# Kernel optimization log

Measured on AMD Instinct MI355X. Metric: run time of the kernel, lower is better.

Reference implementation:

```python
import jax, jax.numpy as jnp
import numpy as np
import math

N_HEAD = 8
LN_EPS = 1e-5


def _layernorm(x, w, b):
    # Biased variance as in the triton kernel: var = E[x^2] - mean^2
    mean = jnp.mean(x, axis=-1, keepdims=True)
    var = jnp.mean(x * x, axis=-1, keepdims=True) - mean * mean
    return (x - mean) * jax.lax.rsqrt(var + LN_EPS) * w + b


def _gelu_tanh(x):
    # matches triton gelu: tanh approximation
    return 0.5 * x * (1.0 + jnp.tanh(0.7978845608 * (x + 0.044715 * x * x * x)))


def _causal_attention(qkv, n_head):
    B, T, C3 = qkv.shape
    C = C3 // 3
    D = C // n_head
    q, k, v = jnp.split(qkv, 3, axis=-1)
    q = q.reshape(B, T, n_head, D)
    k = k.reshape(B, T, n_head, D)
    v = v.reshape(B, T, n_head, D)
    scale = 1.0 / math.sqrt(D)
    scores = jnp.einsum('bqhd,bkhd->bhqk', q, k) * scale  # [B,H,T,T]
    causal = jnp.tril(jnp.ones((T, T), dtype=bool))
    scores = jnp.where(causal, scores, -jnp.inf)
    p = jax.nn.softmax(scores, axis=-1)
    out = jnp.einsum('bhqk,bkhd->bqhd', p, v)
    return out.reshape(B, T, C)


def setup_inputs() -> dict:
    key = jax.random.key(0)
    ks = jax.random.split(key, 8)
    B, T, C = 8, 2048, 768
    s = 0.02
    return {
        'x': jax.random.normal(ks[0], (B, T, C), jnp.float32),
        'ln1_w': jnp.ones((C,), jnp.float32),
        'ln1_b': jnp.zeros((C,), jnp.float32),
        'w_qkv': jax.random.normal(ks[1], (3 * C, C), jnp.float32) * s,
        'b_qkv': jnp.zeros((3 * C,), jnp.float32),
        'w_attn_proj': jax.random.normal(ks[2], (C, C), jnp.float32) * s,
        'b_attn_proj': jnp.zeros((C,), jnp.float32),
        'ln2_w': jnp.ones((C,), jnp.float32),
        'ln2_b': jnp.zeros((C,), jnp.float32),
        'w_fc': jax.random.normal(ks[3], (4 * C, C), jnp.float32) * s,
        'b_fc': jnp.zeros((4 * C,), jnp.float32),
        'w_mlp_proj': jax.random.normal(ks[4], (C, 4 * C), jnp.float32) * s,
        'b_mlp_proj': jnp.zeros((C,), jnp.float32),
    }


def reference(x, ln1_w, ln1_b, w_qkv, b_qkv, w_attn_proj, b_attn_proj,
              ln2_w, ln2_b, w_fc, b_fc, w_mlp_proj, b_mlp_proj):
    # attention block: fused LN + QKV linear, causal flash attention, out proj, residual
    qkv = _layernorm(x, ln1_w, ln1_b) @ w_qkv.T + b_qkv          # [B,T,3C]
    att = _causal_attention(qkv, N_HEAD)                          # [B,T,C]
    x = x + (att @ w_attn_proj.T + b_attn_proj)
    # MLP block: fused LN + fc + gelu, proj, residual
    h = _gelu_tanh(_layernorm(x, ln2_w, ln2_b) @ w_fc.T + b_fc)   # [B,T,4C]
    x = x + (h @ w_mlp_proj.T + b_mlp_proj)
    return x
```

## Files before the change

kernel.cpp:

```cpp
#include <hip/hip_runtime.h>
#include <hip/hip_bf16.h>
#include <cstdint>
#include <cstddef>

typedef __attribute__((ext_vector_type(8))) short bf16x8;
typedef __attribute__((ext_vector_type(4))) short bf16x4;
typedef __attribute__((ext_vector_type(4))) float f32x4;
typedef __attribute__((ext_vector_type(16))) float f32x16;

#define GLB_AS(p) ((const __attribute__((address_space(1))) void*)(p))
#define LDS_AS(p) ((__attribute__((address_space(3))) void*)(p))

__device__ __forceinline__ short f2bf(float f) {
    union { float f; unsigned u; } x; x.f = f;
    unsigned r = (x.u + 0x7fffu + ((x.u >> 16) & 1u)) >> 16;
    return (short)r;
}
__device__ __forceinline__ unsigned packbf2(float a, float b) {
    union { float f; unsigned u; } x, y; x.f = a; y.f = b;
    return (x.u >> 16) | (y.u & 0xffff0000u);
}
__device__ __forceinline__ f32x4 MF(bf16x8 a, bf16x8 b, f32x4 c) {
    return __builtin_amdgcn_mfma_f32_16x16x32_bf16(a, b, c, 0, 0, 0);
}
__device__ __forceinline__ f32x16 MF32(bf16x8 a, bf16x8 b, f32x16 c) {
    return __builtin_amdgcn_mfma_f32_32x32x16_bf16(a, b, c, 0, 0, 0);
}

__global__ __launch_bounds__(256) void k_cast4(const float* __restrict__ s0,
                                               const float* __restrict__ s1,
                                               const float* __restrict__ s2,
                                               const float* __restrict__ s3,
                                               short* __restrict__ d0,
                                               short* __restrict__ d1,
                                               short* __restrict__ d2,
                                               short* __restrict__ d3,
                                               int n0, int n1, int n2, int n3) {
    const int total = n0 + n1 + n2 + n3;
    int i = blockIdx.x * 256 + threadIdx.x;
    const int stride = gridDim.x * 256;
    for (; i < total; i += stride) {
        int j = i;
        const float* s; short* d;
        if (j < n0) { s = s0; d = d0; }
        else {
            j -= n0;
            if (j < n1) { s = s1; d = d1; }
            else {
                j -= n1;
                if (j < n2) { s = s2; d = d2; }
                else { j -= n2; s = s3; d = d3; }
            }
        }
        float4 v = ((const float4*)s)[j];
        bf16x4 o;
        o[0] = f2bf(v.x); o[1] = f2bf(v.y); o[2] = f2bf(v.z); o[3] = f2bf(v.w);
        ((bf16x4*)d)[j] = o;
    }
}

__global__ __launch_bounds__(256) void k_layernorm(const float* __restrict__ x,
                                                   const float* __restrict__ w,
                                                   const float* __restrict__ b,
                                                   short* __restrict__ out) {
    const int row = blockIdx.x;
    const int tid = threadIdx.x;
    const float* xr = x + (size_t)row * 768;
    float v0 = xr[tid], v1 = xr[tid + 256], v2 = xr[tid + 512];
    float s = v0 + v1 + v2;
    float ss = v0 * v0 + v1 * v1 + v2 * v2;
    #pragma unroll
    for (int m = 32; m; m >>= 1) { s += __shfl_xor(s, m); ss += __shfl_xor(ss, m); }
    __shared__ float red[8];
    int wid = tid >> 6, lane = tid & 63;
    if (lane == 0) { red[wid] = s; red[4 + wid] = ss; }
    __syncthreads();
    s = red[0] + red[1] + red[2] + red[3];
    ss = red[4] + red[5] + red[6] + red[7];
    float mean = s * (1.f / 768.f);
    float var = ss * (1.f / 768.f) - mean * mean;
    float inv = rsqrtf(var + 1e-5f);
    short* orow = out + (size_t)row * 768;
    orow[tid]       = f2bf((v0 - mean) * inv * w[tid]       + b[tid]);
    orow[tid + 256] = f2bf((v1 - mean) * inv * w[tid + 256] + b[tid + 256]);
    orow[tid + 512] = f2bf((v2 - mean) * inv * w[tid + 512] + b[tid + 512]);
}

template <int EPI, int NFR>
__global__ __launch_bounds__(512, 2) void k_gemm256(const short* __restrict__ A,
                                                    const short* __restrict__ B,
                                                    const float* __restrict__ bias,
                                                    const float* __restrict__ res,
                                                    void* __restrict__ out,
                                                    int M, int N, int K) {
    __shared__ short As2[2][256 * 64];
    __shared__ short Bs2[2][NFR * 64 * 64];
    const int tid = threadIdx.x, lane = tid & 63, wid = tid >> 6;
    const int l4 = lane & 15, lh = lane >> 4;
    const int wm = wid >> 2, wn = wid & 3;
    const int gx = gridDim.x;
    const int nwg = gx * gridDim.y;
    int wg = blockIdx.y * gx + blockIdx.x;
    { const int q = nwg >> 3; wg = (wg & 7) * q + (wg >> 3); }
    const int row0 = (wg / gx) * 256, col0 = (wg % gx) * (NFR * 64);

    auto stageA = [&](short* lds, int mh, int k0) {
        #pragma unroll
        for (int i = 0; i < 2; ++i) {
            const int chunk = wid * 2 + i;
            const int dl = mh * 16384 + chunk * 1024 + lane * 16;
            const int r = dl >> 7;
            const int cb = (dl & 127) ^ ((r & 7) << 4);
            __builtin_amdgcn_global_load_lds(
                GLB_AS(A + (size_t)(row0 + r) * K + k0 + (cb >> 1)),
                LDS_AS(lds + mh * 8192 + chunk * 512), 16, 0, 0);
        }
    };
    auto stageB = [&](short* lds, int k0) {
        #pragma unroll
        for (int i = 0; i < NFR; ++i) {
            const int chunk = wid * NFR + i;
            const int dl = chunk * 1024 + lane * 16;
            const int r = dl >> 7;
            const int cb = (dl & 127) ^ ((r & 7) << 4);
            __builtin_amdgcn_global_load_lds(
                GLB_AS(B + (size_t)(col0 + r) * K + k0 + (cb >> 1)),
                LDS_AS(lds + chunk * 512), 16, 0, 0);
        }
    };
    auto rd = [&](const short* lds, int r, int kb) -> bf16x8 {
        return *(const bf16x8*)((const char*)lds + r * 128 +
                                ((kb * 64 + lh * 16) ^ ((r & 7) << 4)));
    };

    f32x4 acc[8][NFR] = {};
    bf16x8 a[4][2], b0[2][2], b1[2][2];
    const int NT = K >> 6;

    stageA(As2[0], 0, 0);
    stageA(As2[0], 1, 0);
    stageB(Bs2[0], 0);
    asm volatile("s_waitcnt vmcnt(0)" ::: "memory");
    __builtin_amdgcn_s_barrier();

    for (int t = 0; t < NT; ++t) {
        const int cur = t & 1, nxt = cur ^ 1;
        const short* Ac = As2[cur];
        const short* Bc = Bs2[cur];
        const int kn = (t + 1) << 6;
        const bool more = (t + 1 < NT);
        #pragma unroll
        for (int mi = 0; mi < 4; ++mi) {
            const int r = wm * 128 + mi * 16 + l4;
            a[mi][0] = rd(Ac, r, 0); a[mi][1] = rd(Ac, r, 1);
        }
        #pragma unroll
        for (int ni = 0; ni < 2; ++ni) {
            const int r = wn * (NFR * 16) + ni * 16 + l4;
            b0[ni][0] = rd(Bc, r, 0); b0[ni][1] = rd(Bc, r, 1);
        }
        if (more) { stageA(As2[nxt], 0, kn); stageA(As2[nxt], 1, kn); }
        __builtin_amdgcn_s_setprio(1);
        #pragma unroll
        for (int mi = 0; mi < 4; ++mi)
            #pragma unroll
            for (int ni = 0; ni < 2; ++ni) {
                acc[mi][ni] = MF(a[mi][0], b0[ni][0], acc[mi][ni]);
                acc[mi][ni] = MF(a[mi][1], b0[ni][1], acc[mi][ni]);
            }
        __builtin_amdgcn_s_setprio(0);
        __builtin_amdgcn_s_barrier();
        #pragma unroll
        for (int j = 0; j < NFR - 2; ++j) {
            const int r = wn * (NFR * 16) + (2 + j) * 16 + l4;
            b1[j][0] = rd(Bc, r, 0); b1[j][1] = rd(Bc, r, 1);
        }
        if (more) stageB(Bs2[nxt], kn);
        __builtin_amdgcn_s_setprio(1);
        #pragma unroll
        for (int mi = 0; mi < 4; ++mi)
            #pragma unroll
            for (int j = 0; j < NFR - 2; ++j) {
                acc[mi][2 + j] = MF(a[mi][0], b1[j][0], acc[mi][2 + j]);
                acc[mi][2 + j] = MF(a[mi][1], b1[j][1], acc[mi][2 + j]);
            }
        __builtin_amdgcn_s_setprio(0);
        __builtin_amdgcn_s_barrier();
        #pragma unroll
        for (int mi = 0; mi < 4; ++mi) {
            const int r = wm * 128 + (4 + mi) * 16 + l4;
            a[mi][0] = rd(Ac, r, 0); a[mi][1] = rd(Ac, r, 1);
        }
        __builtin_amdgcn_s_setprio(1);
        #pragma unroll
        for (int mi = 0; mi < 4; ++mi)
            #pragma unroll
            for (int j = 0; j < NFR - 2; ++j) {
                acc[4 + mi][2 + j] = MF(a[mi][0], b1[j][0], acc[4 + mi][2 + j]);
                acc[4 + mi][2 + j] = MF(a[mi][1], b1[j][1], acc[4 + mi][2 + j]);
            }
        __builtin_amdgcn_s_setprio(0);
        __builtin_amdgcn_s_barrier();
        __builtin_amdgcn_s_setprio(1);
        #pragma unroll
        for (int mi = 0; mi < 4; ++mi)
            #pragma unroll
            for (int ni = 0; ni < 2; ++ni) {
                acc[4 + mi][ni] = MF(a[mi][0], b0[ni][0], acc[4 + mi][ni]);
                acc[4 + mi][ni] = MF(a[mi][1], b0[ni][1], acc[4 + mi][ni]);
            }
        __builtin_amdgcn_s_setprio(0);
        asm volatile("s_waitcnt vmcnt(0)" ::: "memory");
        __builtin_amdgcn_s_barrier();
    }

    #pragma unroll
    for (int mi = 0; mi < 8; ++mi) {
        const int rowb = row0 + wm * 128 + mi * 16 + lh * 4;
        #pragma unroll
        for (int ni = 0; ni < NFR; ++ni) {
            const int col = col0 + wn * (NFR * 16) + ni * 16 + l4;
            const float bv = bias[col];
            #pragma unroll
            for (int j = 0; j < 4; ++j) {
                const size_t idx = (size_t)(rowb + j) * N + col;
                float v = acc[mi][ni][j] + bv;
                if (EPI == 0) {
                    ((short*)out)[idx] = f2bf(v);
                } else if (EPI == 1) {
                    ((float*)out)[idx] = v + res[idx];
                } else {
                    float u = v + 0.044715f * v * v * v;
                    float t = 1.f - 2.f / (__expf(1.5957691216f * u) + 1.f);
                    ((short*)out)[idx] = f2bf(0.5f * v * (1.f + t));
                }
            }
        }
    }
}

__global__ __launch_bounds__(256, 2) void k_attn6(const short* __restrict__ qkv,
                                                  short* __restrict__ att) {
    __shared__ short Ks[2][64 * 128];
    __shared__ short Vs[2][96 * 64];
    const int tid = threadIdx.x, lane = tid & 63, wid = tid >> 6;
    const int lq = lane & 31, hi = lane >> 5;
    const int h = blockIdx.y, b = blockIdx.z;
    const short* base = qkv + (size_t)b * 2048 * 2304 + h * 96;
    const short* Kb = base + 768;
    const short* Vb = base + 1536;
    const int vkvr = (tid / 12) * 4, vd0 = (tid % 12) * 8;
    const int vslot = (vkvr & ~12) | ((vkvr & 4) << 1) | ((vkvr & 8) >> 1);
    bf16x8 vreg[4];
    const float QSC = 0.14724445f;

    auto stageK = [&](int jt, int bb) {
        const int kv0 = jt * 64;
        for (int c = wid; c < 16; c += 4) {
            const int dl = c * 1024 + lane * 16;
            const int row = dl >> 8;
            const int scol = (dl & 255) ^ ((row & 7) << 4);
            __builtin_amdgcn_global_load_lds(GLB_AS(Kb + (size_t)(kv0 + row) * 2304 + (scol >> 1)),
                                             LDS_AS(&Ks[bb][c * 512]), 16, 0, 0);
        }
    };
    auto loadV = [&](int jt) {
        if (tid < 192) {
            const int kv0 = jt * 64;
            #pragma unroll
            for (int e = 0; e < 4; ++e)
                vreg[e] = *(const bf16x8*)(Vb + (size_t)(kv0 + vkvr + e) * 2304 + vd0);
        }
    };
    auto writeV = [&](int bb) {
        if (tid < 192) {
            #pragma unroll
            for (int f = 0; f < 8; ++f) {
                const int row = vd0 + f;
                const int sw = ((row & 7) ^ ((row >> 3) & 7)) << 4;
                const int byte = (row * 128 + vslot * 2) ^ sw;
                bf16x4 w4;
                w4[0] = vreg[0][f]; w4[1] = vreg[1][f]; w4[2] = vreg[2][f]; w4[3] = vreg[3][f];
                *(bf16x4*)((char*)&Vs[bb][0] + byte) = w4;
            }
        }
    };

    for (int half = 0; half < 2; ++half) {
        const int qt = half ? 15 - (int)blockIdx.x : (int)blockIdx.x;
        const int q0 = qt * 128 + wid * 32;
        const int qa = q0 + lq;

        bf16x8 qf[6];
        #pragma unroll
        for (int kb = 0; kb < 6; ++kb) {
            bf16x8 v = *(const bf16x8*)(base + (size_t)qa * 2304 + kb * 16 + hi * 8);
            #pragma unroll
            for (int e = 0; e < 8; ++e) {
                union { unsigned u; float f; } x;
                x.u = ((unsigned)(unsigned short)v[e]) << 16;
                qf[kb][e] = f2bf(x.f * QSC);
            }
        }

        f32x16 o[3] = {};
        float lrow = 0.f;
        const int nt = 2 * qt + 2;

        stageK(0, 0);
        loadV(0);
        asm volatile("s_waitcnt vmcnt(0)" ::: "memory");
        writeV(0);
        __syncthreads();

        int cur = 0;
        for (int jt = 0; jt < nt; ++jt) {
            const int nxt = cur ^ 1;
            const bool more = (jt + 1 < nt);
            if (more) { stageK(jt + 1, nxt); loadV(jt + 1); }

            const int kv0 = jt * 64;
            if (kv0 <= q0 + 31) {
                const bool full = (kv0 + 63 <= q0);
                f32x16 s0 = {}, s1 = {};
                #pragma unroll
                for (int kb = 0; kb < 6; ++kb) {
                    const int r0 = lq, r1 = 32 + lq;
                    bf16x8 kf0 = *(const bf16x8*)((const char*)&Ks[cur][0] +
                                  r0 * 256 + ((kb * 32 + hi * 16) ^ ((r0 & 7) << 4)));
                    bf16x8 kf1 = *(const bf16x8*)((const char*)&Ks[cur][0] +
                                  r1 * 256 + ((kb * 32 + hi * 16) ^ ((r1 & 7) << 4)));
                    s0 = MF32(kf0, qf[kb], s0);
                    s1 = MF32(kf1, qf[kb], s1);
                }
                if (!full) {
                    #pragma unroll
                    for (int r = 0; r < 16; ++r) {
                        const int kvl = (r & 3) + 8 * (r >> 2) + 4 * hi;
                        if (kv0 + kvl > qa) s0[r] = -INFINITY;
                        if (kv0 + 32 + kvl > qa) s1[r] = -INFINITY;
                    }
                }
                #pragma unroll
                for (int r = 0; r < 16; ++r) {
                    s0[r] = exp2f(s0[r]);
                    s1[r] = exp2f(s1[r]);
                }
                float ar[16];
                #pragma unroll
                for (int r = 0; r < 16; ++r) ar[r] = s0[r] + s1[r];
                #pragma unroll
                for (int st = 8; st; st >>= 1)
                    #pragma unroll
                    for (int r = 0; r < 8; ++r)
                        if (r < st) ar[r] += ar[r + st];
                lrow += ar[0] + __shfl_xor(ar[0], 32);
                unsigned pk0[8], pk1[8];
                #pragma unroll
                for (int j = 0; j < 8; ++j) {
                    pk0[j] = packbf2(s0[2 * j], s0[2 * j + 1]);
                    pk1[j] = packbf2(s1[2 * j], s1[2 * j + 1]);
                }
                #pragma unroll
                for (int db = 0; db < 3; ++db) {
                    const int vrow = db * 32 + lq;
                    const int vsw = ((vrow & 7) ^ ((vrow >> 3) & 7)) << 4;
                    #pragma unroll
                    for (int c = 0; c < 4; ++c) {
                        bf16x8 vf = *(const bf16x8*)((const char*)&Vs[cur][0] +
                                     vrow * 128 + ((c * 32 + hi * 16) ^ vsw));
                        union { unsigned u[4]; bf16x8 v; } pa;
                        const unsigned* pk = (c < 2) ? pk0 : pk1;
                        const int o4 = (c & 1) * 4;
                        pa.u[0] = pk[o4]; pa.u[1] = pk[o4 + 1];
                        pa.u[2] = pk[o4 + 2]; pa.u[3] = pk[o4 + 3];
                        o[db] = MF32(vf, pa.v, o[db]);
                    }
                }
            }

            if (more) {
                asm volatile("s_waitcnt vmcnt(0)" ::: "memory");
                writeV(nxt);
            }
            __syncthreads();
            cur = nxt;
        }

        const float inv = 1.f / lrow;
        short* orow = att + (size_t)((size_t)b * 2048 + qa) * 768 + h * 96;
        #pragma unroll
        for (int db = 0; db < 3; ++db)
            #pragma unroll
            for (int j = 0; j < 4; ++j) {
                bf16x4 ov;
                #pragma unroll
                for (int e = 0; e < 4; ++e) ov[e] = f2bf(o[db][4 * j + e] * inv);
                *(bf16x4*)(orow + db * 32 + 8 * j + 4 * hi) = ov;
            }
    }
}

extern "C" void kernel_launch(void* const* d_in, const int* in_sizes, int n_in,
                              void* d_out, int out_size, void* d_ws, size_t ws_size,
                              hipStream_t stream) {
    (void)in_sizes; (void)n_in; (void)out_size; (void)ws_size;
    const float* x      = (const float*)d_in[0];
    const float* ln1_w  = (const float*)d_in[1];
    const float* ln1_b  = (const float*)d_in[2];
    const float* w_qkv  = (const float*)d_in[3];
    const float* b_qkv  = (const float*)d_in[4];
    const float* w_proj = (const float*)d_in[5];
    const float* b_proj = (const float*)d_in[6];
    const float* ln2_w  = (const float*)d_in[7];
    const float* ln2_b  = (const float*)d_in[8];
    const float* w_fc   = (const float*)d_in[9];
    const float* b_fc   = (const float*)d_in[10];
    const float* w_mlp  = (const float*)d_in[11];
    const float* b_mlp  = (const float*)d_in[12];

    const int C = 768, M = 8 * 2048;

    char* ws = (char*)d_ws;
    size_t off = 0;
    auto alloc = [&](size_t bytes) {
        char* p = ws + off;
        off += (bytes + 255) & ~(size_t)255;
        return p;
    };
    short* wqkv_b = (short*)alloc((size_t)3 * C * C * 2);
    short* wproj_b = (short*)alloc((size_t)C * C * 2);
    short* wfc_b  = (short*)alloc((size_t)4 * C * C * 2);
    short* wmlp_b = (short*)alloc((size_t)4 * C * C * 2);
    short* bufA   = (short*)alloc((size_t)M * C * 2);
    short* bufB   = (short*)alloc((size_t)M * 4 * C * 2);
    float* x2     = (float*)alloc((size_t)M * C * 4);

    k_cast4<<<dim3(1728), dim3(256), 0, stream>>>(
        w_qkv, w_proj, w_fc, w_mlp, wqkv_b, wproj_b, wfc_b, wmlp_b,
        3 * C * C / 4, C * C / 4, 4 * C * C / 4, 4 * C * C / 4);

    k_layernorm<<<dim3(M), dim3(256), 0, stream>>>(x, ln1_w, ln1_b, bufA);
    k_gemm256<0, 3><<<dim3(2304 / 192, M / 256), dim3(512), 0, stream>>>(
        bufA, wqkv_b, b_qkv, nullptr, bufB, M, 2304, C);
    k_attn6<<<dim3(8, 8, 8), dim3(256), 0, stream>>>(bufB, bufA);
    k_gemm256<1, 3><<<dim3(768 / 192, M / 256), dim3(512), 0, stream>>>(
        bufA, wproj_b, b_proj, x, x2, M, C, C);
    k_layernorm<<<dim3(M), dim3(256), 0, stream>>>(x2, ln2_w, ln2_b, bufA);
    k_gemm256<2, 4><<<dim3(3072 / 256, M / 256), dim3(512), 0, stream>>>(
        bufA, wfc_b, b_fc, nullptr, bufB, M, 3072, C);
    k_gemm256<1, 3><<<dim3(768 / 192, M / 256), dim3(512), 0, stream>>>(
        bufB, wmlp_b, b_mlp, x2, d_out, M, C, 4 * C);
}
```

Measured before the change: 434.8 us.

## Process paired high/low query tiles in one KV sweep sharing staged K/V

The attention kernel now handles the low and high causal query tiles of a pair together in a single loop over KV tiles, instead of two sequential passes. Each staged K/V tile in LDS is used by both query sets, which roughly halves K/V global loads and syncs for the short tile. It also flattens the grid to 1D with head as the fastest index for better L2 locality, and adds s_setprio around the MFMA sections. In exchange it doubles the live Q fragments and accumulators, which raises register pressure and may cost occupancy or cause spills.

```diff
diff --git a/kernel.cpp b/kernel.cpp
--- a/kernel.cpp
+++ b/kernel.cpp
@@ -239,13 +239,75 @@
     }
 }
 
-__global__ __launch_bounds__(256, 2) void k_attn6(const short* __restrict__ qkv,
+#define ATTN_PROC(QF, O, LROW, QA, Q0)                                         \
+    if (kv0 <= (Q0) + 31) {                                                    \
+        const bool full = (kv0 + 63 <= (Q0));                                  \
+        f32x16 s0 = {}, s1 = {};                                               \
+        __builtin_amdgcn_s_setprio(1);                                         \
+        _Pragma("unroll")                                                      \
+        for (int kb = 0; kb < 6; ++kb) {                                       \
+            const int r0 = lq, r1 = 32 + lq;                                   \
+            bf16x8 kf0 = *(const bf16x8*)((const char*)&Ks[cur][0] +           \
+                          r0 * 256 + ((kb * 32 + hi * 16) ^ ((r0 & 7) << 4))); \
+            bf16x8 kf1 = *(const bf16x8*)((const char*)&Ks[cur][0] +           \
+                          r1 * 256 + ((kb * 32 + hi * 16) ^ ((r1 & 7) << 4))); \
+            s0 = MF32(kf0, QF[kb], s0);                                        \
+            s1 = MF32(kf1, QF[kb], s1);                                        \
+        }                                                                      \
+        __builtin_amdgcn_s_setprio(0);                                         \
+        if (!full) {                                                           \
+            _Pragma("unroll")                                                  \
+            for (int r = 0; r < 16; ++r) {                                     \
+                const int kvl = (r & 3) + 8 * (r >> 2) + 4 * hi;               \
+                if (kv0 + kvl > (QA)) s0[r] = -INFINITY;                       \
+                if (kv0 + 32 + kvl > (QA)) s1[r] = -INFINITY;                  \
+            }                                                                  \
+        }                                                                      \
+        _Pragma("unroll")                                                      \
+        for (int r = 0; r < 16; ++r) { s0[r] = exp2f(s0[r]); s1[r] = exp2f(s1[r]); } \
+        float ar[16];                                                          \
+        _Pragma("unroll")                                                      \
+        for (int r = 0; r < 16; ++r) ar[r] = s0[r] + s1[r];                    \
+        _Pragma("unroll")                                                      \
+        for (int st = 8; st; st >>= 1)                                         \
+            _Pragma("unroll")                                                  \
+            for (int r = 0; r < 8; ++r)                                        \
+                if (r < st) ar[r] += ar[r + st];                               \
+        (LROW) += ar[0] + __shfl_xor(ar[0], 32);                               \
+        unsigned pk0[8], pk1[8];                                               \
+        _Pragma("unroll")                                                      \
+        for (int j = 0; j < 8; ++j) {                                          \
+            pk0[j] = packbf2(s0[2 * j], s0[2 * j + 1]);                        \
+            pk1[j] = packbf2(s1[2 * j], s1[2 * j + 1]);                        \
+        }                                                                      \
+        __builtin_amdgcn_s_setprio(1);                                         \
+        _Pragma("unroll")                                                      \
+        for (int db = 0; db < 3; ++db) {                                       \
+            const int vrow = db * 32 + lq;                                     \
+            const int vsw = ((vrow & 7) ^ ((vrow >> 3) & 7)) << 4;             \
+            _Pragma("unroll")                                                  \
+            for (int c = 0; c < 4; ++c) {                                      \
+                bf16x8 vf = *(const bf16x8*)((const char*)&Vs[cur][0] +        \
+                             vrow * 128 + ((c * 32 + hi * 16) ^ vsw));         \
+                union { unsigned u[4]; bf16x8 v; } pa;                         \
+                const unsigned* pk = (c < 2) ? pk0 : pk1;                      \
+                const int o4 = (c & 1) * 4;                                    \
+                pa.u[0] = pk[o4]; pa.u[1] = pk[o4 + 1];                        \
+                pa.u[2] = pk[o4 + 2]; pa.u[3] = pk[o4 + 3];                    \
+                (O)[db] = MF32(vf, pa.v, (O)[db]);                             \
+            }                                                                  \
+        }                                                                      \
+        __builtin_amdgcn_s_setprio(0);                                         \
+    }
+
+__global__ __launch_bounds__(256, 2) void k_attn8(const short* __restrict__ qkv,
                                                   short* __restrict__ att) {
     __shared__ short Ks[2][64 * 128];
     __shared__ short Vs[2][96 * 64];
     const int tid = threadIdx.x, lane = tid & 63, wid = tid >> 6;
     const int lq = lane & 31, hi = lane >> 5;
-    const int h = blockIdx.y, b = blockIdx.z;
+    const int L = blockIdx.x;
+    const int h = L & 7, bx = (L >> 3) & 7, b = L >> 6;
     const short* base = qkv + (size_t)b * 2048 * 2304 + h * 96;
     const short* Kb = base + 768;
     const short* Vb = base + 1536;
@@ -286,116 +348,76 @@
         }
     };
 
-    for (int half = 0; half < 2; ++half) {
-        const int qt = half ? 15 - (int)blockIdx.x : (int)blockIdx.x;
-        const int q0 = qt * 128 + wid * 32;
-        const int qa = q0 + lq;
-
-        bf16x8 qf[6];
-        #pragma unroll
-        for (int kb = 0; kb < 6; ++kb) {
-            bf16x8 v = *(const bf16x8*)(base + (size_t)qa * 2304 + kb * 16 + hi * 8);
-            #pragma unroll
-            for (int e = 0; e < 8; ++e) {
-                union { unsigned u; float f; } x;
-                x.u = ((unsigned)(unsigned short)v[e]) << 16;
-                qf[kb][e] = f2bf(x.f * QSC);
-            }
-        }
-
-        f32x16 o[3] = {};
-        float lrow = 0.f;
-        const int nt = 2 * qt + 2;
-
-        stageK(0, 0);
-        loadV(0);
-        asm volatile("s_waitcnt vmcnt(0)" ::: "memory");
-        writeV(0);
+    const int qtH = 15 - bx, qtL = bx;
+    const int q0H = qtH * 128 + wid * 32, q0L = qtL * 128 + wid * 32;
+    const int qaH = q0H + lq, qaL = q0L + lq;
+
+    bf16x8 qfH[6], qfL[6];
+    #pragma unroll
+    for (int kb = 0; kb < 6; ++kb) {
+        bf16x8 vH = *(const bf16x8*)(base + (size_t)qaH * 2304 + kb * 16 + hi * 8);
+        bf16x8 vL = *(const bf16x8*)(base + (size_t)qaL * 2304 + kb * 16 + hi * 8);
+        #pragma unroll
+        for (int e = 0; e < 8; ++e) {
+            union { unsigned u; float f; } x, y;
+            x.u = ((unsigned)(unsigned short)vH[e]) << 16;
+            y.u = ((unsigned)(unsigned short)vL[e]) << 16;
+            qfH[kb][e] = f2bf(x.f * QSC);
+            qfL[kb][e] = f2bf(y.f * QSC);
+        }
+    }
+
+    f32x16 oH[3] = {}, oL[3] = {};
+    float lrowH = 0.f, lrowL = 0.f;
+    const int nt = 2 * qtH + 2;
+
+    stageK(0, 0);
+    loadV(0);
+    asm volatile("s_waitcnt vmcnt(0)" ::: "memory");
+    writeV(0);
+    __syncthreads();
+
+    int cur = 0;
+    for (int jt = 0; jt < nt; ++jt) {
+        const int nxt = cur ^ 1;
+        const bool more = (jt + 1 < nt);
+        if (more) { stageK(jt + 1, nxt); loadV(jt + 1); }
+
+        const int kv0 = jt * 64;
+        ATTN_PROC(qfH, oH, lrowH, qaH, q0H)
+        ATTN_PROC(qfL, oL, lrowL, qaL, q0L)
+
+        if (more) {
+            asm volatile("s_waitcnt vmcnt(0)" ::: "memory");
+            writeV(nxt);
+        }
         __syncthreads();
-
-        int cur = 0;
-        for (int jt = 0; jt < nt; ++jt) {
-            const int nxt = cur ^ 1;
-            const bool more = (jt + 1 < nt);
-            if (more) { stageK(jt + 1, nxt); loadV(jt + 1); }
-
-            const int kv0 = jt * 64;
-            if (kv0 <= q0 + 31) {
-                const bool full = (kv0 + 63 <= q0);
-                f32x16 s0 = {}, s1 = {};
-                #pragma unroll
-                for (int kb = 0; kb < 6; ++kb) {
-                    const int r0 = lq, r1 = 32 + lq;
-                    bf16x8 kf0 = *(const bf16x8*)((const char*)&Ks[cur][0] +
-                                  r0 * 256 + ((kb * 32 + hi * 16) ^ ((r0 & 7) << 4)));
-                    bf16x8 kf1 = *(const bf16x8*)((const char*)&Ks[cur][0] +
-                                  r1 * 256 + ((kb * 32 + hi * 16) ^ ((r1 & 7) << 4)));
-                    s0 = MF32(kf0, qf[kb], s0);
-                    s1 = MF32(kf1, qf[kb], s1);
-                }
-                if (!full) {
-                    #pragma unroll
-                    for (int r = 0; r < 16; ++r) {
-                        const int kvl = (r & 3) + 8 * (r >> 2) + 4 * hi;
-                        if (kv0 + kvl > qa) s0[r] = -INFINITY;
-                        if (kv0 + 32 + kvl > qa) s1[r] = -INFINITY;
-                    }
-                }
-                #pragma unroll
-                for (int r = 0; r < 16; ++r) {
-                    s0[r] = exp2f(s0[r]);
-                    s1[r] = exp2f(s1[r]);
-                }
-                float ar[16];
-                #pragma unroll
-                for (int r = 0; r < 16; ++r) ar[r] = s0[r] + s1[r];
-                #pragma unroll
-                for (int st = 8; st; st >>= 1)
-                    #pragma unroll
-                    for (int r = 0; r < 8; ++r)
-                        if (r < st) ar[r] += ar[r + st];
-                lrow += ar[0] + __shfl_xor(ar[0], 32);
-                unsigned pk0[8], pk1[8];
-                #pragma unroll
-                for (int j = 0; j < 8; ++j) {
-                    pk0[j] = packbf2(s0[2 * j], s0[2 * j + 1]);
-                    pk1[j] = packbf2(s1[2 * j], s1[2 * j + 1]);
-                }
-                #pragma unroll
-                for (int db = 0; db < 3; ++db) {
-                    const int vrow = db * 32 + lq;
-                    const int vsw = ((vrow & 7) ^ ((vrow >> 3) & 7)) << 4;
-                    #pragma unroll
-                    for (int c = 0; c < 4; ++c) {
-                        bf16x8 vf = *(const bf16x8*)((const char*)&Vs[cur][0] +
-                                     vrow * 128 + ((c * 32 + hi * 16) ^ vsw));
-                        union { unsigned u[4]; bf16x8 v; } pa;
-                        const unsigned* pk = (c < 2) ? pk0 : pk1;
-                        const int o4 = (c & 1) * 4;
-                        pa.u[0] = pk[o4]; pa.u[1] = pk[o4 + 1];
-                        pa.u[2] = pk[o4 + 2]; pa.u[3] = pk[o4 + 3];
-                        o[db] = MF32(vf, pa.v, o[db]);
-                    }
-                }
-            }
-
-            if (more) {
-                asm volatile("s_waitcnt vmcnt(0)" ::: "memory");
-                writeV(nxt);
-            }
-            __syncthreads();
-            cur = nxt;
-        }
-
-        const float inv = 1.f / lrow;
-        short* orow = att + (size_t)((size_t)b * 2048 + qa) * 768 + h * 96;
+        cur = nxt;
+    }
+
+    {
+        const float inv = 1.f / lrowH;
+        short* orow = att + (size_t)((size_t)b * 2048 + qaH) * 768 + h * 96;
         #pragma unroll
         for (int db = 0; db < 3; ++db)
             #pragma unroll
             for (int j = 0; j < 4; ++j) {
                 bf16x4 ov;
                 #pragma unroll
-                for (int e = 0; e < 4; ++e) ov[e] = f2bf(o[db][4 * j + e] * inv);
+                for (int e = 0; e < 4; ++e) ov[e] = f2bf(oH[db][4 * j + e] * inv);
+                *(bf16x4*)(orow + db * 32 + 8 * j + 4 * hi) = ov;
+            }
+    }
+    {
+        const float inv = 1.f / lrowL;
+        short* orow = att + (size_t)((size_t)b * 2048 + qaL) * 768 + h * 96;
+        #pragma unroll
+        for (int db = 0; db < 3; ++db)
+            #pragma unroll
+            for (int j = 0; j < 4; ++j) {
+                bf16x4 ov;
+                #pragma unroll
+                for (int e = 0; e < 4; ++e) ov[e] = f2bf(oL[db][4 * j + e] * inv);
                 *(bf16x4*)(orow + db * 32 + 8 * j + 4 * hi) = ov;
             }
     }
@@ -443,7 +465,7 @@
     k_layernorm<<<dim3(M), dim3(256), 0, stream>>>(x, ln1_w, ln1_b, bufA);
     k_gemm256<0, 3><<<dim3(2304 / 192, M / 256), dim3(512), 0, stream>>>(
         bufA, wqkv_b, b_qkv, nullptr, bufB, M, 2304, C);
-    k_attn6<<<dim3(8, 8, 8), dim3(256), 0, stream>>>(bufB, bufA);
+    k_attn8<<<dim3(512), dim3(256), 0, stream>>>(bufB, bufA);
     k_gemm256<1, 3><<<dim3(768 / 192, M / 256), dim3(512), 0, stream>>>(
         bufA, wproj_b, b_proj, x, x2, M, C, C);
     k_layernorm<<<dim3(M), dim3(256), 0, stream>>>(x2, ln2_w, ln2_b, bufA);
```

Result: faster. 424.7 us (-2.3%).
